# Kernel tuning notes

Measured on AMD Instinct MI355X. Metric: run time of the kernel, lower is better.

The kernel has to match this reference:

```python
import jax, jax.numpy as jnp
import numpy as np

B, S, E, DQ, DV = 8, 2048, 1024, 128, 128


def setup_inputs() -> dict:
    k0 = jax.random.key(0)
    ks = jax.random.split(k0, 10)
    scale_in = 1.0 / np.sqrt(E)
    return {
        "pad_mask": jax.random.uniform(ks[0], (B, S)) < 0.1,  # True = padded key position
        "query": jax.random.normal(ks[1], (B, S, E), jnp.float32),
        "key": jax.random.normal(ks[2], (B, S, E), jnp.float32),
        "value": jax.random.normal(ks[3], (B, S, E), jnp.float32),
        "Wq": jax.random.uniform(ks[4], (E, DQ), jnp.float32, -scale_in, scale_in),
        "bq": jnp.zeros((DQ,), jnp.float32),
        "Wk": jax.random.uniform(ks[5], (E, DQ), jnp.float32, -scale_in, scale_in),
        "bk": jnp.zeros((DQ,), jnp.float32),
        "Wv": jax.random.uniform(ks[6], (E, DV), jnp.float32, -scale_in, scale_in),
        "bv": jnp.zeros((DV,), jnp.float32),
    }


def reference(pad_mask, query, key, value, Wq, bq, Wk, bk, Wv, bv):
    # Linear projections (torch Linear: x @ W^T + b; weights stored pre-transposed here)
    q = query @ Wq + bq  # [B,S,DQ]
    k = key @ Wk + bk    # [B,S,DQ]
    v = value @ Wv + bv  # [B,S,DV]

    scores = jnp.einsum("bqd,bkd->bqk", q, k)  # [B,S,S]
    # Causal mask applied BEFORE scaling (as in source); -inf/scale is still -inf
    seq = scores.shape[1]
    causal = jnp.triu(jnp.ones((seq, seq), bool), k=1)
    scores = jnp.where(causal[None], -jnp.inf, scores)
    scores = scores / jnp.asarray(q.shape[-1] ** 0.5, scores.dtype)
    # Padding mask: mask key positions with -1e9 (broadcast over query dim)
    scores = jnp.where(pad_mask[:, None, :], jnp.asarray(-1e9, scores.dtype), scores)

    attn = jax.nn.softmax(scores, axis=-1)
    return jnp.einsum("bqk,bkd->bqd", attn, v)  # [B,S,DV]
```

## Files before the change

kernel.cpp:

```cpp
#include <hip/hip_runtime.h>
#include <hip/hip_bf16.h>

#define SEQ 2048
#define EMB 1024
#define DH  128
#define QSCALE 0.08838834764831845f

typedef __attribute__((ext_vector_type(4))) float f32x4;
typedef __attribute__((ext_vector_type(8))) short bf16x8;
typedef __attribute__((ext_vector_type(4))) short bf16x4;

__device__ __forceinline__ short f2bf(float f) {
  unsigned u = __builtin_bit_cast(unsigned, f);
  u += 0x7fffu + ((u >> 16) & 1u);
  return (short)(u >> 16);
}

__device__ __forceinline__ float bf2f(short s) {
  unsigned u = ((unsigned)(unsigned short)s) << 16;
  return __builtin_bit_cast(float, u);
}

__device__ __forceinline__ f32x4 mfma16(bf16x8 a, bf16x8 b, f32x4 c) {
  return __builtin_amdgcn_mfma_f32_16x16x32_bf16(a, b, c, 0, 0, 0);
}

__device__ __forceinline__ void gl_lds16(void* lds_base, const void* gsrc) {
  __builtin_amdgcn_global_load_lds(
      (const __attribute__((address_space(1))) void*)gsrc,
      (__attribute__((address_space(3))) void*)lds_base, 16, 0, 0);
}

__global__ void prep_weights(const float* __restrict__ Wq, const float* __restrict__ Wk,
                             const float* __restrict__ Wv, short* __restrict__ wt) {
  int gid = blockIdx.x * 256 + threadIdx.x;
  int lane = gid & 63, c = lane & 15, g = (lane >> 4) & 3;
  int nb = (gid >> 6) & 7;
  int kk = (gid >> 9) & 31;
  int p = gid >> 14;
  const float* W = (p == 0) ? Wq : ((p == 1) ? Wk : Wv);
  bf16x8 v;
#pragma unroll
  for (int j = 0; j < 8; ++j)
    v[j] = f2bf(W[(kk * 32 + g * 8 + j) * DH + nb * 16 + c]);
  *(bf16x8*)(&wt[(size_t)gid * 8]) = v;
}

__global__ __launch_bounds__(256, 3) void proj_gemm(
    const float* __restrict__ Xq, const float* __restrict__ Xk, const float* __restrict__ Xv,
    const short* __restrict__ wt,
    const float* __restrict__ bq, const float* __restrict__ bk, const float* __restrict__ bv,
    short* __restrict__ qp, short* __restrict__ kp, short* __restrict__ vt) {
  __shared__ char abuf[3][8192];
  __shared__ char wbuf[3][8192];

  const int tid = threadIdx.x;
  const int w = tid >> 6, lane = tid & 63;
  const int g = lane >> 4, c = lane & 15;
  const int bid = blockIdx.x;
  const int p = bid >> 8, mb = bid & 255;
  const int row0 = mb << 6;
  const int k0 = (bid * 5) & 31;
  const float* X    = (p == 0) ? Xq : ((p == 1) ? Xk : Xv);
  const float* bias = (p == 0) ? bq : ((p == 1) ? bk : bv);
  const char* Xb  = (const char*)X;
  const char* Wtb = (const char*)wt + (size_t)p * 262144;

  f32x4 acc[8];
#pragma unroll
  for (int nb = 0; nb < 8; ++nb) acc[nb] = (f32x4){0.f, 0.f, 0.f, 0.f};

  auto stage = [&](int buf, int kk) {
#pragma unroll
    for (int i = 0; i < 2; ++i) {
      int ch = w + i * 4;
      int phys = ch * 1024 + lane * 16;
      int lg = phys ^ (((phys >> 7) & 7) << 4);
      gl_lds16(abuf[buf] + ch * 1024,
               Xb + (size_t)(row0 + (lg >> 7)) * 4096 + kk * 128 + (lg & 127));
    }
#pragma unroll
    for (int i = 0; i < 2; ++i) {
      int ch = w + i * 4;
      gl_lds16(wbuf[buf] + ch * 1024,
               Wtb + (size_t)kk * 8192 + ch * 1024 + lane * 16);
    }
  };

  auto compute = [&](int buf) {
    const char* ab = abuf[buf];
    const char* wb = wbuf[buf];
    bf16x8 wfr[8];
#pragma unroll
    for (int nb = 0; nb < 8; ++nb)
      wfr[nb] = *(const bf16x8*)(wb + nb * 1024 + lane * 16);
    int r = (w << 4) + c;
    int ad = (r << 7) + ((g << 5) ^ ((r & 7) << 4));
    f32x4 lo = *(const f32x4*)(ab + ad);
    f32x4 hi = *(const f32x4*)(ab + (ad ^ 16));
    bf16x8 a;
#pragma unroll
    for (int j = 0; j < 4; ++j) { a[j] = f2bf(lo[j]); a[4 + j] = f2bf(hi[j]); }
#pragma unroll
    for (int nb = 0; nb < 8; ++nb) acc[nb] = mfma16(a, wfr[nb], acc[nb]);
  };

  stage(0, k0);
  int bufc = 0;
#pragma unroll 1
  for (int t = 0; t < 32; ++t) {
    int nbuf = (bufc == 2) ? 0 : bufc + 1;
    if (t + 1 < 32) {
      stage(nbuf, (k0 + t + 1) & 31);
      asm volatile("s_waitcnt vmcnt(4)" ::: "memory");
    } else {
      asm volatile("s_waitcnt vmcnt(0)" ::: "memory");
    }
    __builtin_amdgcn_s_barrier();
    __builtin_amdgcn_sched_barrier(0);
    compute(bufc);
    bufc = nbuf;
  }

  float bvals[8];
#pragma unroll
  for (int nb = 0; nb < 8; ++nb) bvals[nb] = bias[nb * 16 + c];

  if (p < 2) {
    short* outp = (p == 0) ? qp : kp;
    float sc = (p == 0) ? QSCALE : 1.0f;
#pragma unroll
    for (int r = 0; r < 4; ++r) {
      int token = row0 + (w << 4) + g * 4 + r;
#pragma unroll
      for (int nb = 0; nb < 8; ++nb)
        outp[token * 128 + nb * 16 + c] = f2bf((acc[nb][r] + bvals[nb]) * sc);
    }
  } else {
    int tok0 = row0 + (w << 4) + g * 4;
    int b_ = tok0 >> 11, s_ = tok0 & 2047;
#pragma unroll
    for (int nb = 0; nb < 8; ++nb) {
      int col = nb * 16 + c;
      bf16x4 v4;
#pragma unroll
      for (int r = 0; r < 4; ++r) v4[r] = f2bf(acc[nb][r] + bvals[nb]);
      *(bf16x4*)(&vt[((size_t)(b_ * 128 + col)) * 2048 + s_]) = v4;
    }
  }
}

__global__ __launch_bounds__(256) void avgv2_kernel(
    const short* __restrict__ vt, const int* __restrict__ pad,
    const float* __restrict__ bvv, float* __restrict__ avgv) {
  int b = blockIdx.x >> 3, dg = blockIdx.x & 7;
  int t = threadIdx.x, doff = t >> 4, sl = t & 15;
  int d = dg * 16 + doff;
  const short* vrow = vt + ((size_t)(b * 128 + d)) * 2048 + sl * 128;
  const int* prow = pad + (b << 11) + sl * 128;
  float sum = 0.f;
  int cnt = 0;
  for (int i = 0; i < 16; ++i) {
    bf16x8 v8 = *(const bf16x8*)(vrow + i * 8);
#pragma unroll
    for (int j = 0; j < 8; ++j) {
      int pd = prow[i * 8 + j];
      cnt += (pd != 0);
      if (pd) sum += bf2f(v8[j]);
    }
  }
#pragma unroll
  for (int xm = 1; xm < 16; xm <<= 1) {
    sum += __shfl_xor(sum, xm, 64);
    cnt += __shfl_xor(cnt, xm, 64);
  }
  if (sl == 0) avgv[(b << 7) + d] = (cnt > 0) ? (sum / (float)cnt) : 0.f;
  (void)bvv;
}

__device__ __forceinline__ void stage_kv(short* kb, short* vb,
                                         const char* kb_base, const char* vb_base,
                                         int kt, int w, int lane) {
#pragma unroll
  for (int ch = w; ch < 16; ch += 4) {
    int phys = ch * 1024 + lane * 16;
    int lg = phys ^ (((phys >> 8) & 7) << 4);
    gl_lds16((char*)kb + ch * 1024,
             kb_base + (size_t)(kt * 64 + (lg >> 8)) * 256 + (lg & 255));
  }
#pragma unroll
  for (int ch = w; ch < 16; ch += 4) {
    int phys = ch * 1024 + lane * 16;
    int lg = phys ^ (((phys >> 7) & 7) << 4);
    gl_lds16((char*)vb + ch * 1024,
             vb_base + (size_t)(lg >> 7) * 4096 + kt * 128 + (lg & 127));
  }
}

template <bool CAUSAL>
__device__ __forceinline__ void attn_tile(
    const short* __restrict__ k_lds, const short* __restrict__ v_lds, short* __restrict__ p_w,
    const bf16x8 (&qf)[4], f32x4 (&acc_o)[8], float (&m_r)[4], float (&l_r)[4],
    const int* __restrict__ padp, int kt, int qrow_g, int g, int c) {
  f32x4 sc[4];
#pragma unroll
  for (int nb = 0; nb < 4; ++nb) sc[nb] = (f32x4){0.f, 0.f, 0.f, 0.f};
#pragma unroll
  for (int ks = 0; ks < 4; ++ks) {
    bf16x8 kf[4];
#pragma unroll
    for (int nb = 0; nb < 4; ++nb) {
      int n = (nb << 4) + c;
      int off = (n << 8) + (ks << 6) + (g << 4);
      kf[nb] = *(const bf16x8*)((const char*)k_lds + (off ^ ((n & 7) << 4)));
    }
#pragma unroll
    for (int nb = 0; nb < 4; ++nb) sc[nb] = mfma16(qf[ks], kf[nb], sc[nb]);
  }

  int padv[4];
#pragma unroll
  for (int nb = 0; nb < 4; ++nb) padv[nb] = padp[kt + (nb << 4) + c];
  float sv[4][4];
#pragma unroll
  for (int nb = 0; nb < 4; ++nb) {
    bool pd = padv[nb] != 0;
    int key = kt + (nb << 4) + c;
#pragma unroll
    for (int r = 0; r < 4; ++r) {
      float s = sc[nb][r];
      if (CAUSAL && key > qrow_g + r) s = -1e30f;
      if (pd) s = -1e30f;
      sv[nb][r] = s;
    }
  }
  float tmax[4];
#pragma unroll
  for (int r = 0; r < 4; ++r)
    tmax[r] = fmaxf(fmaxf(sv[0][r], sv[1][r]), fmaxf(sv[2][r], sv[3][r]));
#pragma unroll
  for (int xm = 1; xm < 16; xm <<= 1)
#pragma unroll
    for (int r = 0; r < 4; ++r) tmax[r] = fmaxf(tmax[r], __shfl_xor(tmax[r], xm, 64));
  float al[4];
#pragma unroll
  for (int r = 0; r < 4; ++r) {
    float mn = fmaxf(m_r[r], tmax[r]);
    al[r] = __expf(m_r[r] - mn);
    m_r[r] = mn;
  }
  float ls[4] = {0.f, 0.f, 0.f, 0.f};
#pragma unroll
  for (int nb = 0; nb < 4; ++nb)
#pragma unroll
    for (int r = 0; r < 4; ++r) {
      float pp = __expf(sv[nb][r] - m_r[r]);
      sv[nb][r] = pp;
      ls[r] += pp;
    }
#pragma unroll
  for (int xm = 1; xm < 16; xm <<= 1)
#pragma unroll
    for (int r = 0; r < 4; ++r) ls[r] += __shfl_xor(ls[r], xm, 64);
#pragma unroll
  for (int r = 0; r < 4; ++r) l_r[r] = l_r[r] * al[r] + ls[r];
#pragma unroll
  for (int nb = 0; nb < 8; ++nb)
#pragma unroll
    for (int r = 0; r < 4; ++r) acc_o[nb][r] *= al[r];

#pragma unroll
  for (int nb = 0; nb < 4; ++nb)
#pragma unroll
    for (int r = 0; r < 4; ++r)
      p_w[(g * 4 + r) * 72 + (nb << 4) + c] = f2bf(sv[nb][r]);

#pragma unroll
  for (int ks = 0; ks < 2; ++ks) {
    bf16x8 pa = *(const bf16x8*)((const char*)p_w + c * 144 + ks * 64 + g * 16);
#pragma unroll
    for (int nb = 0; nb < 8; ++nb) {
      int n = (nb << 4) + c;
      int off = (n << 7) + (ks << 6) + (g << 4);
      bf16x8 vf = *(const bf16x8*)((const char*)v_lds + (off ^ ((n & 7) << 4)));
      acc_o[nb] = mfma16(pa, vf, acc_o[nb]);
    }
  }
}

__global__ __launch_bounds__(256) void flash_attn(
    const short* __restrict__ qp, const short* __restrict__ kp, const short* __restrict__ vt,
    const int* __restrict__ pad, float* __restrict__ partO, float* __restrict__ partML) {
  __shared__ short k_lds[2][64 * 128];
  __shared__ short v_lds[2][128 * 64];
  __shared__ short p_lds[4][16 * 72];
  const int tid = threadIdx.x, w = tid >> 6, lane = tid & 63;
  const int g = lane >> 4, c = lane & 15;
  const int j = blockIdx.x;
  int b, qi, half;
  if (j < 256) { b = j >> 5; qi = j & 31; half = 0; }
  else { int u = j - 256; b = u >> 5; qi = 31 - (u & 31); half = 1; }
  const int T = qi + 1;
  const int t0 = half ? (T >> 1) : 0;
  const int t1 = half ? T : (T >> 1);
  const int q0 = qi << 6;

  bf16x8 qf[4];
  {
    int token = (b << 11) + q0 + (w << 4) + c;
    const char* qrow = (const char*)qp + (size_t)token * 256;
#pragma unroll
    for (int s = 0; s < 4; ++s) qf[s] = *(const bf16x8*)(qrow + s * 64 + g * 16);
  }
  f32x4 acc_o[8];
#pragma unroll
  for (int i = 0; i < 8; ++i) acc_o[i] = (f32x4){0.f, 0.f, 0.f, 0.f};
  float m_r[4] = {-1e30f, -1e30f, -1e30f, -1e30f};
  float l_r[4] = {0.f, 0.f, 0.f, 0.f};

  const char* kb_base = (const char*)kp + (size_t)(b << 11) * 256;
  const char* vb_base = (const char*)vt + (size_t)b * 524288;
  const int* padp = pad + (b << 11);
  const int qrow_g = q0 + (w << 4) + (g << 2);

  if (t1 > t0) {
    stage_kv(k_lds[0], v_lds[0], kb_base, vb_base, t0, w, lane);
    __syncthreads();
    int cur = 0;
    for (int t = t0; t < t1; ++t) {
      if (t + 1 < t1)
        stage_kv(k_lds[cur ^ 1], v_lds[cur ^ 1], kb_base, vb_base, t + 1, w, lane);
      if (half && t == T - 1)
        attn_tile<true>(k_lds[cur], v_lds[cur], p_lds[w], qf, acc_o, m_r, l_r,
                        padp, t << 6, qrow_g, g, c);
      else
        attn_tile<false>(k_lds[cur], v_lds[cur], p_lds[w], qf, acc_o, m_r, l_r,
                         padp, t << 6, qrow_g, g, c);
      __syncthreads();
      cur ^= 1;
    }
  }

  float* pO = partO + (size_t)j * (64 * 128);
  float* pML = partML + (size_t)j * 128;
#pragma unroll
  for (int nb = 0; nb < 8; ++nb)
#pragma unroll
    for (int r = 0; r < 4; ++r)
      pO[(w * 16 + g * 4 + r) * 128 + (nb << 4) + c] = acc_o[nb][r];
  if (c == 0)
#pragma unroll
    for (int r = 0; r < 4; ++r) {
      pML[(w * 16 + g * 4 + r) * 2] = m_r[r];
      pML[(w * 16 + g * 4 + r) * 2 + 1] = l_r[r];
    }
}

__global__ __launch_bounds__(256) void combine_kernel(
    const float* __restrict__ partO, const float* __restrict__ partML,
    const float* __restrict__ avgv, float* __restrict__ out) {
  int gid = blockIdx.x * 256 + threadIdx.x;
  int row = gid >> 5;
  int d4 = gid & 31;
  int b = row >> 11, s = row & 2047;
  int qt = s >> 6, lr = s & 63;
  int wid1 = (b << 5) + qt;
  int wid2 = 256 + (b << 5) + (31 - qt);
  float m1 = partML[wid1 * 128 + lr * 2], l1 = partML[wid1 * 128 + lr * 2 + 1];
  float m2 = partML[wid2 * 128 + lr * 2], l2 = partML[wid2 * 128 + lr * 2 + 1];
  float m = fmaxf(m1, m2);
  f32x4 o;
  if (m < -1e8f) {
    o = *(const f32x4*)(avgv + (b << 7) + (d4 << 2));
  } else {
    float f1 = __expf(m1 - m), f2 = __expf(m2 - m);
    float inv = 1.0f / (l1 * f1 + l2 * f2);
    f32x4 o1 = *(const f32x4*)(partO + ((size_t)wid1 * 64 + lr) * 128 + (d4 << 2));
    f32x4 o2 = *(const f32x4*)(partO + ((size_t)wid2 * 64 + lr) * 128 + (d4 << 2));
#pragma unroll
    for (int k = 0; k < 4; ++k) o[k] = (o1[k] * f1 + o2[k] * f2) * inv;
  }
  *(f32x4*)(out + (size_t)row * 128 + (d4 << 2)) = o;
}

extern "C" void kernel_launch(void* const* d_in, const int* in_sizes, int n_in,
                              void* d_out, int out_size, void* d_ws, size_t ws_size,
                              hipStream_t stream) {
  const int*   pad   = (const int*)d_in[0];
  const float* query = (const float*)d_in[1];
  const float* key   = (const float*)d_in[2];
  const float* value = (const float*)d_in[3];
  const float* Wq    = (const float*)d_in[4];
  const float* bq    = (const float*)d_in[5];
  const float* Wk    = (const float*)d_in[6];
  const float* bk    = (const float*)d_in[7];
  const float* Wv    = (const float*)d_in[8];
  const float* bv    = (const float*)d_in[9];
  char* ws = (char*)d_ws;
  short* wt    = (short*)ws;
  short* qp    = (short*)(ws + 786432);
  short* kp    = (short*)(ws + 4980736);
  short* vt    = (short*)(ws + 9175040);
  float* partO = (float*)(ws + 13369344);
  float* partML= (float*)(ws + 30146560);
  float* avgv  = (float*)(ws + 30408704);
  float* out   = (float*)d_out;

  prep_weights<<<dim3(192), dim3(256), 0, stream>>>(Wq, Wk, Wv, wt);
  proj_gemm<<<dim3(768), dim3(256), 0, stream>>>(query, key, value, wt, bq, bk, bv, qp, kp, vt);
  avgv2_kernel<<<dim3(64), dim3(256), 0, stream>>>(vt, pad, bv, avgv);
  flash_attn<<<dim3(512), dim3(256), 0, stream>>>(qp, kp, vt, pad, partO, partML);
  combine_kernel<<<dim3(2048), dim3(256), 0, stream>>>(partO, partML, avgv, out);
}
```

Baseline: 96.80 us.

## Load projection A operand directly to registers instead of staging via LDS

The projection GEMM no longer stages the fp32 activation tile through shared memory. Each lane loads its A fragment straight from global memory into registers, double-buffered across an unrolled-by-two loop, while only the bf16 weights still go through the triple-buffered LDS ring. Weight fragments are now read from LDS just before each MFMA instead of all up front. This removes the LDS write/read round trip and half the shared memory, but the direct global loads are less coalesced, 32-byte accesses on 4 KB-strided rows, and the staggered per-block k start offset is dropped, which could raise contention on the same weight slices.

```diff
diff --git a/kernel.cpp b/kernel.cpp
--- a/kernel.cpp
+++ b/kernel.cpp
@@ -51,7 +51,6 @@
     const short* __restrict__ wt,
     const float* __restrict__ bq, const float* __restrict__ bk, const float* __restrict__ bv,
     short* __restrict__ qp, short* __restrict__ kp, short* __restrict__ vt) {
-  __shared__ char abuf[3][8192];
   __shared__ char wbuf[3][8192];
 
   const int tid = threadIdx.x;
@@ -59,67 +58,70 @@
   const int g = lane >> 4, c = lane & 15;
   const int bid = blockIdx.x;
   const int p = bid >> 8, mb = bid & 255;
-  const int row0 = mb << 6;
-  const int k0 = (bid * 5) & 31;
+  const int row0 = (mb << 6) + (w << 4);
   const float* X    = (p == 0) ? Xq : ((p == 1) ? Xk : Xv);
   const float* bias = (p == 0) ? bq : ((p == 1) ? bk : bv);
-  const char* Xb  = (const char*)X;
-  const char* Wtb = (const char*)wt + (size_t)p * 262144;
+  const char* Ap = (const char*)X + (size_t)(row0 + c) * 4096 + (g << 5);
+  const char* WT = (const char*)wt + (size_t)p * 262144;
 
   f32x4 acc[8];
 #pragma unroll
   for (int nb = 0; nb < 8; ++nb) acc[nb] = (f32x4){0.f, 0.f, 0.f, 0.f};
 
-  auto stage = [&](int buf, int kk) {
-#pragma unroll
-    for (int i = 0; i < 2; ++i) {
-      int ch = w + i * 4;
-      int phys = ch * 1024 + lane * 16;
-      int lg = phys ^ (((phys >> 7) & 7) << 4);
-      gl_lds16(abuf[buf] + ch * 1024,
-               Xb + (size_t)(row0 + (lg >> 7)) * 4096 + kk * 128 + (lg & 127));
-    }
+  f32x4 aA0, aA1, aB0, aB1;
+
+  auto loadA = [&](f32x4& a0, f32x4& a1, int t) {
+    a0 = *(const f32x4*)(Ap + t * 128);
+    a1 = *(const f32x4*)(Ap + t * 128 + 16);
+  };
+
+  auto stageW = [&](int buf, int t) {
 #pragma unroll
     for (int i = 0; i < 2; ++i) {
       int ch = w + i * 4;
       gl_lds16(wbuf[buf] + ch * 1024,
-               Wtb + (size_t)kk * 8192 + ch * 1024 + lane * 16);
+               WT + (size_t)t * 8192 + ch * 1024 + lane * 16);
     }
   };
 
-  auto compute = [&](int buf) {
-    const char* ab = abuf[buf];
-    const char* wb = wbuf[buf];
-    bf16x8 wfr[8];
-#pragma unroll
-    for (int nb = 0; nb < 8; ++nb)
-      wfr[nb] = *(const bf16x8*)(wb + nb * 1024 + lane * 16);
-    int r = (w << 4) + c;
-    int ad = (r << 7) + ((g << 5) ^ ((r & 7) << 4));
-    f32x4 lo = *(const f32x4*)(ab + ad);
-    f32x4 hi = *(const f32x4*)(ab + (ad ^ 16));
+  auto computeT = [&](const f32x4& a0, const f32x4& a1, int buf) {
     bf16x8 a;
 #pragma unroll
-    for (int j = 0; j < 4; ++j) { a[j] = f2bf(lo[j]); a[4 + j] = f2bf(hi[j]); }
-#pragma unroll
-    for (int nb = 0; nb < 8; ++nb) acc[nb] = mfma16(a, wfr[nb], acc[nb]);
+    for (int j = 0; j < 4; ++j) { a[j] = f2bf(a0[j]); a[4 + j] = f2bf(a1[j]); }
+#pragma unroll
+    for (int nb = 0; nb < 8; ++nb) {
+      bf16x8 wfr = *(const bf16x8*)(wbuf[buf] + nb * 1024 + lane * 16);
+      acc[nb] = mfma16(a, wfr, acc[nb]);
+    }
   };
 
-  stage(0, k0);
-  int bufc = 0;
+  loadA(aA0, aA1, 0);
+  stageW(0, 0);
+  __builtin_amdgcn_sched_barrier(0);
+
 #pragma unroll 1
-  for (int t = 0; t < 32; ++t) {
-    int nbuf = (bufc == 2) ? 0 : bufc + 1;
-    if (t + 1 < 32) {
-      stage(nbuf, (k0 + t + 1) & 31);
+  for (int t = 0; t < 32; t += 2) {
+    loadA(aB0, aB1, t + 1);
+    stageW((t + 1) % 3, t + 1);
+    __builtin_amdgcn_sched_barrier(0);
+    asm volatile("s_waitcnt vmcnt(4)" ::: "memory");
+    __builtin_amdgcn_sched_barrier(0);
+    __builtin_amdgcn_s_barrier();
+    computeT(aA0, aA1, t % 3);
+    __builtin_amdgcn_sched_barrier(0);
+
+    if (t + 2 < 32) {
+      loadA(aA0, aA1, t + 2);
+      stageW((t + 2) % 3, t + 2);
+      __builtin_amdgcn_sched_barrier(0);
       asm volatile("s_waitcnt vmcnt(4)" ::: "memory");
     } else {
       asm volatile("s_waitcnt vmcnt(0)" ::: "memory");
     }
+    __builtin_amdgcn_sched_barrier(0);
     __builtin_amdgcn_s_barrier();
+    computeT(aB0, aB1, (t + 1) % 3);
     __builtin_amdgcn_sched_barrier(0);
-    compute(bufc);
-    bufc = nbuf;
   }
 
   float bvals[8];
@@ -131,13 +133,13 @@
     float sc = (p == 0) ? QSCALE : 1.0f;
 #pragma unroll
     for (int r = 0; r < 4; ++r) {
-      int token = row0 + (w << 4) + g * 4 + r;
+      int token = row0 + g * 4 + r;
 #pragma unroll
       for (int nb = 0; nb < 8; ++nb)
         outp[token * 128 + nb * 16 + c] = f2bf((acc[nb][r] + bvals[nb]) * sc);
     }
   } else {
-    int tok0 = row0 + (w << 4) + g * 4;
+    int tok0 = row0 + g * 4;
     int b_ = tok0 >> 11, s_ = tok0 & 2047;
 #pragma unroll
     for (int nb = 0; nb < 8; ++nb) {
```

Measured after the change: 98.54 us. About the same (+1.8%).
